# Kernel tuning notes

Measured on AMD Instinct MI355X. Metric: run time of the kernel, lower is better.

The kernel has to match this reference:

```python
import jax, jax.numpy as jnp
import numpy as np

BINS = 256

def setup_inputs() -> dict:
    key = jax.random.key(0)
    x = jax.random.normal(key, (64, 3, 512, 512), dtype=jnp.float32)
    return {"x": x}

def reference(x):
    bins = BINS

    def equalize_one(img):
        # img: (C, H, W) -- flattened wholesale, matching the torch per-index loop
        flat = img.reshape(-1)
        mn = flat.min()
        mx = flat.max()
        norm = (flat - mn) * (bins - 1) / (mx - mn + 1e-8)
        norm = jnp.clip(norm, 0, bins - 1)
        idx = norm.astype(jnp.int32)  # bucket index per pixel
        hist = jnp.zeros((bins,), jnp.float32).at[idx].add(1.0)  # bincount
        cdf = jnp.cumsum(hist)
        cdf_norm = (cdf - cdf.min()) / (cdf.max() - cdf.min() + 1e-8)
        return cdf_norm[idx].reshape(img.shape)  # gather equalized values

    return jax.vmap(equalize_one)(x)
```

## Files before the change

### kernel.cpp

```cpp
#include <hip/hip_runtime.h>

#define NUM_BINS 256
#define NPI (3*512*512)
#define TPB 256
#define MMX_BLOCKS 32
#define MM_BLOCKS 16
#define GB_PER_IMG 32
#define NSUB 32
#define SUBSTRIDE 257
#define G_VEC 8

typedef float f32x4 __attribute__((ext_vector_type(4)));

__device__ __forceinline__ int bin_of(float v, float mn, float denom) {
  float norm = (v - mn) * 255.0f / denom;
  norm = fminf(fmaxf(norm, 0.0f), 255.0f);
  return (int)norm;
}

__device__ __forceinline__ unsigned pack4(int b0, int b1, int b2, int b3) {
  return (unsigned)b0 | ((unsigned)b1 << 8) | ((unsigned)b2 << 16) | ((unsigned)b3 << 24);
}

__global__ void minmax_k(const float4* __restrict__ x,
                         float* __restrict__ mmn, float* __restrict__ mmx) {
  const int chunk4 = NPI / 4 / MMX_BLOCKS;
  int img = blockIdx.x / MMX_BLOCKS;
  int blk = blockIdx.x % MMX_BLOCKS;
  const float4* p = x + (size_t)img * (NPI/4) + (size_t)blk * chunk4;
  float mn = 3.4e38f, mx = -3.4e38f;
  #pragma unroll 4
  for (int i = threadIdx.x; i < chunk4; i += TPB) {
    float4 v = p[i];
    mn = fminf(mn, fminf(fminf(v.x, v.y), fminf(v.z, v.w)));
    mx = fmaxf(mx, fmaxf(fmaxf(v.x, v.y), fmaxf(v.z, v.w)));
  }
  for (int off = 32; off > 0; off >>= 1) {
    mn = fminf(mn, __shfl_down(mn, off));
    mx = fmaxf(mx, __shfl_down(mx, off));
  }
  __shared__ float smn[4], smx[4];
  int wave = threadIdx.x >> 6, lane = threadIdx.x & 63;
  if (lane == 0) { smn[wave] = mn; smx[wave] = mx; }
  __syncthreads();
  if (threadIdx.x == 0) {
    mmn[blockIdx.x] = fminf(fminf(smn[0], smn[1]), fminf(smn[2], smn[3]));
    mmx[blockIdx.x] = fmaxf(fmaxf(smx[0], smx[1]), fmaxf(smx[2], smx[3]));
  }
}

__device__ __forceinline__ void load_minmax(const float* __restrict__ mmn,
                                            const float* __restrict__ mmx,
                                            int img, float* s_mn, float* s_dn) {
  if (threadIdx.x < MMX_BLOCKS) {
    float a = mmn[img * MMX_BLOCKS + threadIdx.x];
    float b = mmx[img * MMX_BLOCKS + threadIdx.x];
    for (int off = MMX_BLOCKS / 2; off > 0; off >>= 1) {
      a = fminf(a, __shfl_down(a, off));
      b = fmaxf(b, __shfl_down(b, off));
    }
    if (threadIdx.x == 0) { *s_mn = a; *s_dn = b - a + 1e-8f; }
  }
}

__global__ void hist_k(const float4* __restrict__ x,
                       const float* __restrict__ mmn, const float* __restrict__ mmx,
                       int* __restrict__ histblk, unsigned* __restrict__ bins32) {
  __shared__ int sh[NSUB * SUBSTRIDE];
  __shared__ float s_mn, s_dn;
  load_minmax(mmn, mmx, blockIdx.x / MM_BLOCKS, &s_mn, &s_dn);
  for (int i = threadIdx.x; i < NSUB * SUBSTRIDE; i += TPB) sh[i] = 0;
  const int chunk4 = NPI / 4 / MM_BLOCKS;
  int img = blockIdx.x / MM_BLOCKS;
  int blk = blockIdx.x % MM_BLOCKS;
  __syncthreads();
  float mn = s_mn, denom = s_dn;
  size_t gbase = (size_t)img * (NPI/4) + (size_t)blk * chunk4;
  const float4* p = x + gbase;
  int* mysub = sh + (threadIdx.x & (NSUB - 1)) * SUBSTRIDE;
  bool wb = (bins32 != nullptr);
  for (int i = threadIdx.x; i < chunk4; i += TPB * 8) {
    float4 v[8];
    #pragma unroll
    for (int k = 0; k < 8; ++k) v[k] = p[i + k * TPB];
    int b[8][4];
    #pragma unroll
    for (int k = 0; k < 8; ++k) {
      b[k][0] = bin_of(v[k].x, mn, denom);
      b[k][1] = bin_of(v[k].y, mn, denom);
      b[k][2] = bin_of(v[k].z, mn, denom);
      b[k][3] = bin_of(v[k].w, mn, denom);
    }
    #pragma unroll
    for (int k = 0; k < 8; ++k) {
      atomicAdd(&mysub[b[k][0]], 1);
      atomicAdd(&mysub[b[k][1]], 1);
      atomicAdd(&mysub[b[k][2]], 1);
      atomicAdd(&mysub[b[k][3]], 1);
    }
    if (wb) {
      #pragma unroll
      for (int k = 0; k < 8; ++k)
        bins32[gbase + i + k * TPB] = pack4(b[k][0], b[k][1], b[k][2], b[k][3]);
    }
  }
  __syncthreads();
  int bin = threadIdx.x;
  int s = 0;
  #pragma unroll
  for (int c = 0; c < NSUB; ++c) s += sh[c * SUBSTRIDE + bin];
  histblk[blockIdx.x * NUM_BINS + bin] = s;
}

__global__ void gather_bins_k(const unsigned* __restrict__ bins32,
                              const int* __restrict__ histblk,
                              float4* __restrict__ out) {
  __shared__ int s[NUM_BINS];
  __shared__ float c[NUM_BINS];
  const int f4pi = NPI / 4;
  const int chunk4 = f4pi / GB_PER_IMG;
  const int ITERS = chunk4 / (TPB * G_VEC);
  int img = blockIdx.x / GB_PER_IMG;
  int blk = blockIdx.x % GB_PER_IMG;
  int t = threadIdx.x;
  int v = 0;
  #pragma unroll
  for (int b = 0; b < MM_BLOCKS; ++b)
    v += histblk[(img * MM_BLOCKS + b) * NUM_BINS + t];
  s[t] = v;
  __syncthreads();
  for (int off = 1; off < NUM_BINS; off <<= 1) {
    int add = (t >= off) ? s[t - off] : 0;
    __syncthreads();
    s[t] += add;
    __syncthreads();
  }
  {
    int cdf = s[t], c0 = s[0], cN = s[NUM_BINS - 1];
    c[t] = (float)(cdf - c0) / ((float)(cN - c0) + 1e-8f);
  }
  __syncthreads();
  size_t base = (size_t)img * f4pi + (size_t)blk * chunk4 + threadIdx.x;
  for (int it = 0; it < ITERS; ++it) {
    size_t b0 = base + (size_t)it * TPB * G_VEC;
    unsigned bv[G_VEC];
    #pragma unroll
    for (int j = 0; j < G_VEC; ++j) bv[j] = bins32[b0 + (size_t)j * TPB];
    #pragma unroll
    for (int j = 0; j < G_VEC; ++j) {
      unsigned b = bv[j];
      f32x4 o;
      o.x = c[b & 255u];
      o.y = c[(b >> 8) & 255u];
      o.z = c[(b >> 16) & 255u];
      o.w = c[b >> 24];
      __builtin_nontemporal_store(o, (f32x4*)&out[b0 + (size_t)j * TPB]);
    }
  }
}

__global__ void scan_k(const int* __restrict__ histblk, float* __restrict__ cdfn) {
  __shared__ int s[NUM_BINS];
  int img = blockIdx.x, t = threadIdx.x;
  int v = 0;
  #pragma unroll
  for (int b = 0; b < MM_BLOCKS; ++b)
    v += histblk[(img * MM_BLOCKS + b) * NUM_BINS + t];
  s[t] = v;
  __syncthreads();
  for (int off = 1; off < NUM_BINS; off <<= 1) {
    int add = (t >= off) ? s[t - off] : 0;
    __syncthreads();
    s[t] += add;
    __syncthreads();
  }
  int cdf = s[t], c0 = s[0], cN = s[NUM_BINS - 1];
  cdfn[img * NUM_BINS + t] = (float)(cdf - c0) / ((float)(cN - c0) + 1e-8f);
}

__global__ void gather_x_k(const float4* __restrict__ x,
                           const float* __restrict__ mmn, const float* __restrict__ mmx,
                           const float* __restrict__ cdfn,
                           float4* __restrict__ out) {
  __shared__ float c[NUM_BINS];
  __shared__ float s_mn, s_dn;
  const int f4pi = NPI / 4;
  const int CHUNK = TPB * 4;
  const int bpi = f4pi / CHUNK;
  int img = blockIdx.x / bpi;
  int blk = blockIdx.x % bpi;
  c[threadIdx.x] = cdfn[img * NUM_BINS + threadIdx.x];
  load_minmax(mmn, mmx, img, &s_mn, &s_dn);
  __syncthreads();
  float mn = s_mn, denom = s_dn;
  size_t base = (size_t)img * f4pi + (size_t)blk * CHUNK + threadIdx.x;
  #pragma unroll
  for (int j = 0; j < 4; ++j) {
    float4 v = x[base + (size_t)j * TPB];
    f32x4 o;
    o.x = c[bin_of(v.x, mn, denom)];
    o.y = c[bin_of(v.y, mn, denom)];
    o.z = c[bin_of(v.z, mn, denom)];
    o.w = c[bin_of(v.w, mn, denom)];
    __builtin_nontemporal_store(o, (f32x4*)&out[base + (size_t)j * TPB]);
  }
}

extern "C" void kernel_launch(void* const* d_in, const int* in_sizes, int n_in,
                              void* d_out, int out_size, void* d_ws, size_t ws_size,
                              hipStream_t stream) {
  const float* x = (const float*)d_in[0];
  float* out = (float*)d_out;
  int B = in_sizes[0] / NPI;

  char* ws = (char*)d_ws;
  float* mmn = (float*)ws;
  float* mmx = mmn + (size_t)B * MMX_BLOCKS;
  int* histblk = (int*)(mmx + (size_t)B * MMX_BLOCKS);
  float* cdfn = (float*)(histblk + (size_t)B * MM_BLOCKS * NUM_BINS);
  unsigned* bins32 = (unsigned*)(cdfn + (size_t)B * NUM_BINS);
  size_t need = (size_t)((char*)bins32 - ws) + (size_t)B * NPI;
  bool use_bins = (ws_size >= need);

  minmax_k<<<B * MMX_BLOCKS, TPB, 0, stream>>>((const float4*)x, mmn, mmx);
  hist_k<<<B * MM_BLOCKS, TPB, 0, stream>>>((const float4*)x, mmn, mmx, histblk,
                                            use_bins ? bins32 : nullptr);
  if (use_bins) {
    gather_bins_k<<<B * GB_PER_IMG, TPB, 0, stream>>>(bins32, histblk, (float4*)out);
  } else {
    scan_k<<<B, NUM_BINS, 0, stream>>>(histblk, cdfn);
    gather_x_k<<<B * (NPI/4/(TPB*4)), TPB, 0, stream>>>((const float4*)x, mmn, mmx, cdfn,
                                                        (float4*)out);
  }
}
```

Baseline: 376.0 us.

## Split CDF scan into separate kernel, unroll minmax loads, use normal stores

Moves the per-image histogram reduction and scan out of gather_bins_k into a dedicated scan_k launch, so each of the 32 gather blocks per image no longer redoes the scan. The minmax loop is fully unrolled with four independent float4 loads per iteration to raise memory-level parallelism. Nontemporal stores in both gather kernels are replaced with plain stores. This adds one extra kernel launch and a global round trip for the CDF table, and dropping the nontemporal hint may change cache behaviour for the large output write.

```diff
diff --git a/kernel.cpp b/kernel.cpp
--- a/kernel.cpp
+++ b/kernel.cpp
@@ -29,11 +29,21 @@
   int blk = blockIdx.x % MMX_BLOCKS;
   const float4* p = x + (size_t)img * (NPI/4) + (size_t)blk * chunk4;
   float mn = 3.4e38f, mx = -3.4e38f;
-  #pragma unroll 4
-  for (int i = threadIdx.x; i < chunk4; i += TPB) {
-    float4 v = p[i];
-    mn = fminf(mn, fminf(fminf(v.x, v.y), fminf(v.z, v.w)));
-    mx = fmaxf(mx, fmaxf(fmaxf(v.x, v.y), fmaxf(v.z, v.w)));
+  #pragma unroll
+  for (int it = 0; it < chunk4 / (TPB * 4); ++it) {
+    int i0 = threadIdx.x + it * TPB * 4;
+    float4 v0 = p[i0];
+    float4 v1 = p[i0 + TPB];
+    float4 v2 = p[i0 + 2*TPB];
+    float4 v3 = p[i0 + 3*TPB];
+    mn = fminf(mn, fminf(fminf(v0.x, v0.y), fminf(v0.z, v0.w)));
+    mx = fmaxf(mx, fmaxf(fmaxf(v0.x, v0.y), fmaxf(v0.z, v0.w)));
+    mn = fminf(mn, fminf(fminf(v1.x, v1.y), fminf(v1.z, v1.w)));
+    mx = fmaxf(mx, fmaxf(fmaxf(v1.x, v1.y), fmaxf(v1.z, v1.w)));
+    mn = fminf(mn, fminf(fminf(v2.x, v2.y), fminf(v2.z, v2.w)));
+    mx = fmaxf(mx, fmaxf(fmaxf(v2.x, v2.y), fmaxf(v2.z, v2.w)));
+    mn = fminf(mn, fminf(fminf(v3.x, v3.y), fminf(v3.z, v3.w)));
+    mx = fmaxf(mx, fmaxf(fmaxf(v3.x, v3.y), fmaxf(v3.z, v3.w)));
   }
   for (int off = 32; off > 0; off >>= 1) {
     mn = fminf(mn, __shfl_down(mn, off));
@@ -112,33 +122,35 @@
   histblk[blockIdx.x * NUM_BINS + bin] = s;
 }
 
+__global__ void scan_k(const int* __restrict__ histblk, float* __restrict__ cdfn) {
+  __shared__ int s[NUM_BINS];
+  int img = blockIdx.x, t = threadIdx.x;
+  int v = 0;
+  #pragma unroll
+  for (int b = 0; b < MM_BLOCKS; ++b)
+    v += histblk[(img * MM_BLOCKS + b) * NUM_BINS + t];
+  s[t] = v;
+  __syncthreads();
+  for (int off = 1; off < NUM_BINS; off <<= 1) {
+    int add = (t >= off) ? s[t - off] : 0;
+    __syncthreads();
+    s[t] += add;
+    __syncthreads();
+  }
+  int cdf = s[t], c0 = s[0], cN = s[NUM_BINS - 1];
+  cdfn[img * NUM_BINS + t] = (float)(cdf - c0) / ((float)(cN - c0) + 1e-8f);
+}
+
 __global__ void gather_bins_k(const unsigned* __restrict__ bins32,
-                              const int* __restrict__ histblk,
+                              const float* __restrict__ cdfn,
                               float4* __restrict__ out) {
-  __shared__ int s[NUM_BINS];
   __shared__ float c[NUM_BINS];
   const int f4pi = NPI / 4;
   const int chunk4 = f4pi / GB_PER_IMG;
   const int ITERS = chunk4 / (TPB * G_VEC);
   int img = blockIdx.x / GB_PER_IMG;
   int blk = blockIdx.x % GB_PER_IMG;
-  int t = threadIdx.x;
-  int v = 0;
-  #pragma unroll
-  for (int b = 0; b < MM_BLOCKS; ++b)
-    v += histblk[(img * MM_BLOCKS + b) * NUM_BINS + t];
-  s[t] = v;
-  __syncthreads();
-  for (int off = 1; off < NUM_BINS; off <<= 1) {
-    int add = (t >= off) ? s[t - off] : 0;
-    __syncthreads();
-    s[t] += add;
-    __syncthreads();
-  }
-  {
-    int cdf = s[t], c0 = s[0], cN = s[NUM_BINS - 1];
-    c[t] = (float)(cdf - c0) / ((float)(cN - c0) + 1e-8f);
-  }
+  c[threadIdx.x] = cdfn[img * NUM_BINS + threadIdx.x];
   __syncthreads();
   size_t base = (size_t)img * f4pi + (size_t)blk * chunk4 + threadIdx.x;
   for (int it = 0; it < ITERS; ++it) {
@@ -149,33 +161,14 @@
     #pragma unroll
     for (int j = 0; j < G_VEC; ++j) {
       unsigned b = bv[j];
-      f32x4 o;
+      float4 o;
       o.x = c[b & 255u];
       o.y = c[(b >> 8) & 255u];
       o.z = c[(b >> 16) & 255u];
       o.w = c[b >> 24];
-      __builtin_nontemporal_store(o, (f32x4*)&out[b0 + (size_t)j * TPB]);
-    }
-  }
-}
-
-__global__ void scan_k(const int* __restrict__ histblk, float* __restrict__ cdfn) {
-  __shared__ int s[NUM_BINS];
-  int img = blockIdx.x, t = threadIdx.x;
-  int v = 0;
-  #pragma unroll
-  for (int b = 0; b < MM_BLOCKS; ++b)
-    v += histblk[(img * MM_BLOCKS + b) * NUM_BINS + t];
-  s[t] = v;
-  __syncthreads();
-  for (int off = 1; off < NUM_BINS; off <<= 1) {
-    int add = (t >= off) ? s[t - off] : 0;
-    __syncthreads();
-    s[t] += add;
-    __syncthreads();
-  }
-  int cdf = s[t], c0 = s[0], cN = s[NUM_BINS - 1];
-  cdfn[img * NUM_BINS + t] = (float)(cdf - c0) / ((float)(cN - c0) + 1e-8f);
+      out[b0 + (size_t)j * TPB] = o;
+    }
+  }
 }
 
 __global__ void gather_x_k(const float4* __restrict__ x,
@@ -197,12 +190,12 @@
   #pragma unroll
   for (int j = 0; j < 4; ++j) {
     float4 v = x[base + (size_t)j * TPB];
-    f32x4 o;
+    float4 o;
     o.x = c[bin_of(v.x, mn, denom)];
     o.y = c[bin_of(v.y, mn, denom)];
     o.z = c[bin_of(v.z, mn, denom)];
     o.w = c[bin_of(v.w, mn, denom)];
-    __builtin_nontemporal_store(o, (f32x4*)&out[base + (size_t)j * TPB]);
+    out[base + (size_t)j * TPB] = o;
   }
 }
 
@@ -225,10 +218,10 @@
   minmax_k<<<B * MMX_BLOCKS, TPB, 0, stream>>>((const float4*)x, mmn, mmx);
   hist_k<<<B * MM_BLOCKS, TPB, 0, stream>>>((const float4*)x, mmn, mmx, histblk,
                                             use_bins ? bins32 : nullptr);
+  scan_k<<<B, NUM_BINS, 0, stream>>>(histblk, cdfn);
   if (use_bins) {
-    gather_bins_k<<<B * GB_PER_IMG, TPB, 0, stream>>>(bins32, histblk, (float4*)out);
+    gather_bins_k<<<B * GB_PER_IMG, TPB, 0, stream>>>(bins32, cdfn, (float4*)out);
   } else {
-    scan_k<<<B, NUM_BINS, 0, stream>>>(histblk, cdfn);
     gather_x_k<<<B * (NPI/4/(TPB*4)), TPB, 0, stream>>>((const float4*)x, mmn, mmx, cdfn,
                                                         (float4*)out);
   }
```

Result: slower. 391.7 us (+4.2%).
